# Performance work log

Measured on AMD Instinct MI355X. Metric: run time of the kernel, lower is better.

The kernel has to match this reference:

```python
import jax, jax.numpy as jnp
import numpy as np

N_ENT = 50000
N_REL = 500
N_EDGE = 800000
D_IN = 100
D_OUT = 100
ALPHA = 0.2  # LeakyReLU negative slope


def setup_inputs() -> dict:
    key = jax.random.key(0)
    k0, k1, k2, k3, k4 = jax.random.split(key, 5)
    entity_embedding = jax.random.normal(k0, (N_ENT, D_IN), dtype=jnp.float32) * 0.1
    relation_embedding = jax.random.normal(k1, (N_REL, D_IN), dtype=jnp.float32) * 0.1
    W = jax.random.normal(k2, (D_IN, D_OUT), dtype=jnp.float32) * 0.1
    edge_index = jax.random.randint(k3, (2, N_EDGE), 0, N_ENT, dtype=jnp.int32)
    edge_type = jax.random.randint(k4, (N_EDGE,), 0, N_REL, dtype=jnp.int32)
    return {
        "entity_embedding": entity_embedding,
        "relation_embedding": relation_embedding,
        "W": W,
        "edge_index": edge_index,
        "edge_type": edge_type,
    }


def reference(entity_embedding, relation_embedding, W, edge_index, edge_type):
    N = entity_embedding.shape[0]
    # project input embeddings with shared W (in_features -> out_features)
    ent = entity_embedding @ W          # [N_ent, D]
    rel = relation_embedding @ W        # [N_rel, D]

    h = edge_index[0]                   # destination / head nodes [E]
    t = edge_index[1]                   # source / tail nodes      [E]

    # TransE edge score: ||h + r - t||_2 per edge
    diff = ent[h] + rel[edge_type] - ent[t]          # [E, D]
    score = jnp.sqrt(jnp.sum(diff * diff, axis=1))   # [E]
    e = jax.nn.leaky_relu(score, negative_slope=ALPHA)

    # scatter-softmax over edges grouped by head node
    seg_max = jax.ops.segment_max(e, h, num_segments=N)         # [N]
    seg_max = jnp.where(jnp.isfinite(seg_max), seg_max, 0.0)    # empty segments -> -inf
    ex = jnp.exp(e - seg_max[h])                                 # [E]
    denom = jax.ops.segment_sum(ex, h, num_segments=N)          # [N]
    att = ex / (denom[h] + 1e-16)                                # [E]

    # message: composition 'sub' of tail embedding and relation, weighted by attention
    msg = (ent[t] - rel[edge_type]) * att[:, None]               # [E, D]
    out = jax.ops.segment_sum(msg, h, num_segments=N)            # [N, D]

    # concat=True -> nonlinearity (ELU, standard GAT behavior)
    return jax.nn.elu(out)
```

## Files before the change

kernel.cpp:

```cpp
#include <hip/hip_runtime.h>
#include <math.h>

#define N_ENT  50000
#define N_REL  500
#define N_EDGE 800000
#define D      100
#define ALPHA  0.2f

#define SCAN_B 256
#define NBLK_SCAN ((N_ENT + SCAN_B - 1) / SCAN_B)

#define PROJ_TPB  256
#define PROJ_RPB  50
#define ENT_BLKS  (N_ENT / PROJ_RPB)
#define REL_BLKS  (N_REL / PROJ_RPB)

__global__ __launch_bounds__(PROJ_TPB) void proj_kernel(const float* __restrict__ Xe,
                                                        const float* __restrict__ Xr,
                                                        const float* __restrict__ W,
                                                        float* __restrict__ Ye,
                                                        float* __restrict__ Yr,
                                                        int* __restrict__ deg) {
    __shared__ float Xs[PROJ_RPB * D];
    __shared__ float P[5][D];
    int t = threadIdx.x;

    const float* X; float* Y; size_t xbase;
    if (blockIdx.x < ENT_BLKS) {
        X = Xe; Y = Ye; xbase = (size_t)blockIdx.x * PROJ_RPB * D;
    } else {
        X = Xr; Y = Yr; xbase = (size_t)(blockIdx.x - ENT_BLKS) * PROJ_RPB * D;
    }

    int half, c;
    if (t < 100)                { half = 0; c = t; }
    else if (t >= 128 && t < 228) { half = 1; c = t - 128; }
    else                        { half = -1; c = 0; }

    if (half < 0) {
        int idx = (t < 128) ? (t - 100) : (28 + (t - 228));
        int j = blockIdx.x * 56 + idx;
        if (j < N_ENT) deg[j] = 0;
    }

    for (int i = t; i < PROJ_RPB * D; i += PROJ_TPB)
        Xs[i] = X[xbase + i];

    float w[52];
    if (half == 0) {
        #pragma unroll
        for (int k = 0; k < 52; ++k) w[k] = W[k * D + c];
    } else if (half == 1) {
        #pragma unroll
        for (int k = 0; k < 48; ++k) w[k] = W[(52 + k) * D + c];
    }
    __syncthreads();

    for (int g = 0; g < 10; ++g) {
        int r0 = g * 5;
        float a[5] = {0.f, 0.f, 0.f, 0.f, 0.f};
        if (half == 0) {
            #pragma unroll
            for (int r = 0; r < 5; ++r) {
                const float4* xr = (const float4*)&Xs[(r0 + r) * D];
                #pragma unroll
                for (int q = 0; q < 13; ++q) {
                    float4 xv = xr[q];
                    a[r] = fmaf(xv.x, w[4*q    ], a[r]);
                    a[r] = fmaf(xv.y, w[4*q + 1], a[r]);
                    a[r] = fmaf(xv.z, w[4*q + 2], a[r]);
                    a[r] = fmaf(xv.w, w[4*q + 3], a[r]);
                }
            }
        } else if (half == 1) {
            #pragma unroll
            for (int r = 0; r < 5; ++r) {
                const float4* xr = (const float4*)&Xs[(r0 + r) * D] + 13;
                #pragma unroll
                for (int q = 0; q < 12; ++q) {
                    float4 xv = xr[q];
                    a[r] = fmaf(xv.x, w[4*q    ], a[r]);
                    a[r] = fmaf(xv.y, w[4*q + 1], a[r]);
                    a[r] = fmaf(xv.z, w[4*q + 2], a[r]);
                    a[r] = fmaf(xv.w, w[4*q + 3], a[r]);
                }
            }
            #pragma unroll
            for (int r = 0; r < 5; ++r) P[r][c] = a[r];
        }
        __syncthreads();
        if (half == 0) {
            #pragma unroll
            for (int r = 0; r < 5; ++r)
                Y[xbase + (size_t)(r0 + r) * D + c] = a[r] + P[r][c];
        }
        __syncthreads();
    }
}

__global__ void degree_kernel(const int* __restrict__ h_idx, int* __restrict__ deg) {
    int e = blockIdx.x * blockDim.x + threadIdx.x;
    if (e < N_EDGE) atomicAdd(&deg[h_idx[e]], 1);
}

__global__ void scan1_kernel(const int* __restrict__ deg, int* __restrict__ bsum) {
    __shared__ int s[SCAN_B];
    int i = blockIdx.x * SCAN_B + threadIdx.x;
    s[threadIdx.x] = (i < N_ENT) ? deg[i] : 0;
    __syncthreads();
    for (int off = SCAN_B / 2; off; off >>= 1) {
        if (threadIdx.x < off) s[threadIdx.x] += s[threadIdx.x + off];
        __syncthreads();
    }
    if (threadIdx.x == 0) bsum[blockIdx.x] = s[0];
}

__global__ void scan2_kernel(const int* __restrict__ bsum, int* __restrict__ boff) {
    __shared__ int s[SCAN_B];
    int tid = threadIdx.x;
    int v = (tid < NBLK_SCAN) ? bsum[tid] : 0;
    s[tid] = v;
    __syncthreads();
    for (int off = 1; off < SCAN_B; off <<= 1) {
        int x = (tid >= off) ? s[tid - off] : 0;
        __syncthreads();
        s[tid] += x;
        __syncthreads();
    }
    if (tid < NBLK_SCAN) boff[tid] = s[tid] - v;
}

__global__ void scan3_kernel(const int* __restrict__ deg, const int* __restrict__ boff,
                             int* __restrict__ rowptr, int* __restrict__ cursor) {
    __shared__ int s[SCAN_B];
    int tid = threadIdx.x;
    int i = blockIdx.x * SCAN_B + tid;
    int v = (i < N_ENT) ? deg[i] : 0;
    s[tid] = v;
    __syncthreads();
    for (int off = 1; off < SCAN_B; off <<= 1) {
        int x = (tid >= off) ? s[tid - off] : 0;
        __syncthreads();
        s[tid] += x;
        __syncthreads();
    }
    int excl = s[tid] - v + boff[blockIdx.x];
    if (i < N_ENT) { rowptr[i] = excl; cursor[i] = excl; }
    if (i == N_ENT - 1) rowptr[N_ENT] = excl + v;
}

__global__ void fill_kernel(const int* __restrict__ h_idx, const int* __restrict__ t_idx,
                            const int* __restrict__ etype, int* __restrict__ cursor,
                            int2* __restrict__ tr_sorted) {
    int e = blockIdx.x * blockDim.x + threadIdx.x;
    if (e >= N_EDGE) return;
    int h = h_idx[e];
    int pos = atomicAdd(&cursor[h], 1);
    tr_sorted[pos] = make_int2(t_idx[e], etype[e]);
}

__device__ __forceinline__ float edge_reduce32(const float4& eh, const float4& v) {
    float dx = eh.x + v.x, dy = eh.y + v.y, dz = eh.z + v.z, dw = eh.w + v.w;
    float s = dx * dx;
    s = fmaf(dy, dy, s);
    s = fmaf(dz, dz, s);
    s = fmaf(dw, dw, s);
    #pragma unroll
    for (int off = 16; off; off >>= 1) s += __shfl_xor(s, off, 32);
    return sqrtf(s);
}

__device__ __forceinline__ void online_update(float sc, const float4& v,
                                              float& m, float& den, float4& acc) {
    float d  = sc - m;
    float e  = __expf(-fabsf(d));
    float scale = (d >= 0.f) ? e : 1.f;
    float ex    = (d >= 0.f) ? 1.f : e;
    m = fmaxf(m, sc);
    den   = den * scale + ex;
    acc.x = acc.x * scale - v.x * ex;
    acc.y = acc.y * scale - v.y * ex;
    acc.z = acc.z * scale - v.z * ex;
    acc.w = acc.w * scale - v.w * ex;
}

__global__ __launch_bounds__(256) void fused_kernel(const float* __restrict__ ent,
                                                    const float* __restrict__ rel,
                                                    const int* __restrict__ rowptr,
                                                    const int2* __restrict__ tr_sorted,
                                                    float* __restrict__ out) {
    int head = blockIdx.x * 8 + (threadIdx.x >> 5);
    int lane = threadIdx.x & 31;
    if (head >= N_ENT) return;
    int beg = rowptr[head], end = rowptr[head + 1];

    float4 eh = make_float4(0.f, 0.f, 0.f, 0.f);
    if (lane < 25) eh = ((const float4*)(ent + (size_t)head * D))[lane];

    float  m   = -INFINITY;
    float  den = 0.f;
    float4 acc = make_float4(0.f, 0.f, 0.f, 0.f);

    int i = beg;
    for (; i + 1 < end; i += 2) {
        int2 e0 = tr_sorted[i];
        int2 e1 = tr_sorted[i + 1];
        float4 v0 = make_float4(0.f, 0.f, 0.f, 0.f);
        float4 v1 = make_float4(0.f, 0.f, 0.f, 0.f);
        if (lane < 25) {
            float4 et0 = ((const float4*)(ent + (size_t)e0.x * D))[lane];
            float4 er0 = ((const float4*)(rel + (size_t)e0.y * D))[lane];
            float4 et1 = ((const float4*)(ent + (size_t)e1.x * D))[lane];
            float4 er1 = ((const float4*)(rel + (size_t)e1.y * D))[lane];
            v0 = make_float4(er0.x - et0.x, er0.y - et0.y, er0.z - et0.z, er0.w - et0.w);
            v1 = make_float4(er1.x - et1.x, er1.y - et1.y, er1.z - et1.z, er1.w - et1.w);
        }
        float sc0 = edge_reduce32(eh, v0);
        float sc1 = edge_reduce32(eh, v1);
        online_update(sc0, v0, m, den, acc);
        online_update(sc1, v1, m, den, acc);
    }
    if (i < end) {
        int2 e0 = tr_sorted[i];
        float4 v = make_float4(0.f, 0.f, 0.f, 0.f);
        if (lane < 25) {
            float4 et = ((const float4*)(ent + (size_t)e0.x * D))[lane];
            float4 er = ((const float4*)(rel + (size_t)e0.y * D))[lane];
            v = make_float4(er.x - et.x, er.y - et.y, er.z - et.z, er.w - et.w);
        }
        float sc = edge_reduce32(eh, v);
        online_update(sc, v, m, den, acc);
    }

    float inv = 1.f / (den + 1e-16f);
    float ox = acc.x * inv, oy = acc.y * inv, oz = acc.z * inv, ow = acc.w * inv;
    ox = ox > 0.f ? ox : expm1f(ox);
    oy = oy > 0.f ? oy : expm1f(oy);
    oz = oz > 0.f ? oz : expm1f(oz);
    ow = ow > 0.f ? ow : expm1f(ow);
    if (lane < 25)
        ((float4*)(out + (size_t)head * D))[lane] = make_float4(ox, oy, oz, ow);
}

extern "C" void kernel_launch(void* const* d_in, const int* in_sizes, int n_in,
                              void* d_out, int out_size, void* d_ws, size_t ws_size,
                              hipStream_t stream) {
    const float* entity_emb = (const float*)d_in[0];
    const float* rel_emb    = (const float*)d_in[1];
    const float* W          = (const float*)d_in[2];
    const int*   edge_index = (const int*)d_in[3];
    const int*   edge_type  = (const int*)d_in[4];
    float*       out        = (float*)d_out;

    const int* h_idx = edge_index;
    const int* t_idx = edge_index + N_EDGE;

    float* ent       = (float*)d_ws;
    float* rel       = ent + (size_t)N_ENT * D;
    int*   deg       = (int*)(rel + (size_t)N_REL * D);
    int*   rowptr    = deg + N_ENT;
    int*   cursor    = rowptr + (N_ENT + 1);
    int*   bsum      = cursor + N_ENT;
    int*   boff      = bsum + SCAN_B;
    int2*  tr_sorted = (int2*)(boff + SCAN_B);

    proj_kernel<<<ENT_BLKS + REL_BLKS, PROJ_TPB, 0, stream>>>(entity_emb, rel_emb,
                                                              W, ent, rel, deg);

    degree_kernel<<<(N_EDGE + 255) / 256, 256, 0, stream>>>(h_idx, deg);
    scan1_kernel<<<NBLK_SCAN, SCAN_B, 0, stream>>>(deg, bsum);
    scan2_kernel<<<1, SCAN_B, 0, stream>>>(bsum, boff);
    scan3_kernel<<<NBLK_SCAN, SCAN_B, 0, stream>>>(deg, boff, rowptr, cursor);
    fill_kernel<<<(N_EDGE + 255) / 256, 256, 0, stream>>>(h_idx, t_idx, edge_type,
                                                          cursor, tr_sorted);

    fused_kernel<<<N_ENT / 8, 256, 0, stream>>>(ent, rel, rowptr, tr_sorted, out);
}
```

Measured before the change: 266.2 us.

## Record per-edge rank during degree count, scatter edges without a second atomic pass

The degree-counting atomics now also save each edge's within-segment rank as a ushort, and this work is merged into the projection kernel as extra blocks. The CSR fill then computes each position as rowptr plus rank instead of doing a second atomicAdd on a cursor array, which removes the cursor writes and the fill-stage atomics. A memset replaces the in-kernel zeroing, adding a rank buffer read/write and relying on per-node degree staying under 65536. Edge order within a segment stays nondeterministic, as before.

```diff
diff --git a/kernel.cpp b/kernel.cpp
--- a/kernel.cpp
+++ b/kernel.cpp
@@ -14,16 +14,36 @@
 #define PROJ_RPB  50
 #define ENT_BLKS  (N_ENT / PROJ_RPB)
 #define REL_BLKS  (N_REL / PROJ_RPB)
-
-__global__ __launch_bounds__(PROJ_TPB) void proj_kernel(const float* __restrict__ Xe,
-                                                        const float* __restrict__ Xr,
-                                                        const float* __restrict__ W,
-                                                        float* __restrict__ Ye,
-                                                        float* __restrict__ Yr,
-                                                        int* __restrict__ deg) {
+#define PROJ_BLKS (ENT_BLKS + REL_BLKS)
+#define RANK_BLKS ((N_EDGE + 1023) / 1024)
+
+__global__ __launch_bounds__(PROJ_TPB) void proj_rank_kernel(const float* __restrict__ Xe,
+                                                             const float* __restrict__ Xr,
+                                                             const float* __restrict__ W,
+                                                             float* __restrict__ Ye,
+                                                             float* __restrict__ Yr,
+                                                             const int* __restrict__ h_idx,
+                                                             int* __restrict__ cnt,
+                                                             unsigned short* __restrict__ rank) {
+    int t = threadIdx.x;
+
+    if (blockIdx.x >= PROJ_BLKS) {
+        int eb = (blockIdx.x - PROJ_BLKS) * 1024 + t * 4;
+        if (eb + 3 < N_EDGE) {
+            int4 h4 = *(const int4*)(h_idx + eb);
+            rank[eb    ] = (unsigned short)atomicAdd(&cnt[h4.x], 1);
+            rank[eb + 1] = (unsigned short)atomicAdd(&cnt[h4.y], 1);
+            rank[eb + 2] = (unsigned short)atomicAdd(&cnt[h4.z], 1);
+            rank[eb + 3] = (unsigned short)atomicAdd(&cnt[h4.w], 1);
+        } else {
+            for (int e = eb; e < N_EDGE; ++e)
+                rank[e] = (unsigned short)atomicAdd(&cnt[h_idx[e]], 1);
+        }
+        return;
+    }
+
     __shared__ float Xs[PROJ_RPB * D];
     __shared__ float P[5][D];
-    int t = threadIdx.x;
 
     const float* X; float* Y; size_t xbase;
     if (blockIdx.x < ENT_BLKS) {
@@ -33,15 +53,9 @@
     }
 
     int half, c;
-    if (t < 100)                { half = 0; c = t; }
+    if (t < 100)                  { half = 0; c = t; }
     else if (t >= 128 && t < 228) { half = 1; c = t - 128; }
-    else                        { half = -1; c = 0; }
-
-    if (half < 0) {
-        int idx = (t < 128) ? (t - 100) : (28 + (t - 228));
-        int j = blockIdx.x * 56 + idx;
-        if (j < N_ENT) deg[j] = 0;
-    }
+    else                          { half = -1; c = 0; }
 
     for (int i = t; i < PROJ_RPB * D; i += PROJ_TPB)
         Xs[i] = X[xbase + i];
@@ -98,15 +112,10 @@
     }
 }
 
-__global__ void degree_kernel(const int* __restrict__ h_idx, int* __restrict__ deg) {
-    int e = blockIdx.x * blockDim.x + threadIdx.x;
-    if (e < N_EDGE) atomicAdd(&deg[h_idx[e]], 1);
-}
-
-__global__ void scan1_kernel(const int* __restrict__ deg, int* __restrict__ bsum) {
+__global__ void scan1_kernel(const int* __restrict__ cnt, int* __restrict__ bsum) {
     __shared__ int s[SCAN_B];
     int i = blockIdx.x * SCAN_B + threadIdx.x;
-    s[threadIdx.x] = (i < N_ENT) ? deg[i] : 0;
+    s[threadIdx.x] = (i < N_ENT) ? cnt[i] : 0;
     __syncthreads();
     for (int off = SCAN_B / 2; off; off >>= 1) {
         if (threadIdx.x < off) s[threadIdx.x] += s[threadIdx.x + off];
@@ -130,12 +139,12 @@
     if (tid < NBLK_SCAN) boff[tid] = s[tid] - v;
 }
 
-__global__ void scan3_kernel(const int* __restrict__ deg, const int* __restrict__ boff,
-                             int* __restrict__ rowptr, int* __restrict__ cursor) {
+__global__ void scan3_kernel(const int* __restrict__ cnt, const int* __restrict__ boff,
+                             int* __restrict__ rowptr) {
     __shared__ int s[SCAN_B];
     int tid = threadIdx.x;
     int i = blockIdx.x * SCAN_B + tid;
-    int v = (i < N_ENT) ? deg[i] : 0;
+    int v = (i < N_ENT) ? cnt[i] : 0;
     s[tid] = v;
     __syncthreads();
     for (int off = 1; off < SCAN_B; off <<= 1) {
@@ -145,17 +154,19 @@
         __syncthreads();
     }
     int excl = s[tid] - v + boff[blockIdx.x];
-    if (i < N_ENT) { rowptr[i] = excl; cursor[i] = excl; }
+    if (i < N_ENT) rowptr[i] = excl;
     if (i == N_ENT - 1) rowptr[N_ENT] = excl + v;
 }
 
-__global__ void fill_kernel(const int* __restrict__ h_idx, const int* __restrict__ t_idx,
-                            const int* __restrict__ etype, int* __restrict__ cursor,
-                            int2* __restrict__ tr_sorted) {
+__global__ void scatter_kernel(const int* __restrict__ h_idx, const int* __restrict__ t_idx,
+                               const int* __restrict__ etype,
+                               const int* __restrict__ rowptr,
+                               const unsigned short* __restrict__ rank,
+                               int2* __restrict__ tr_sorted) {
     int e = blockIdx.x * blockDim.x + threadIdx.x;
     if (e >= N_EDGE) return;
     int h = h_idx[e];
-    int pos = atomicAdd(&cursor[h], 1);
+    int pos = rowptr[h] + (int)rank[e];
     tr_sorted[pos] = make_int2(t_idx[e], etype[e]);
 }
 
@@ -255,24 +266,26 @@
     const int* h_idx = edge_index;
     const int* t_idx = edge_index + N_EDGE;
 
-    float* ent       = (float*)d_ws;
-    float* rel       = ent + (size_t)N_ENT * D;
-    int*   deg       = (int*)(rel + (size_t)N_REL * D);
-    int*   rowptr    = deg + N_ENT;
-    int*   cursor    = rowptr + (N_ENT + 1);
-    int*   bsum      = cursor + N_ENT;
-    int*   boff      = bsum + SCAN_B;
-    int2*  tr_sorted = (int2*)(boff + SCAN_B);
-
-    proj_kernel<<<ENT_BLKS + REL_BLKS, PROJ_TPB, 0, stream>>>(entity_emb, rel_emb,
-                                                              W, ent, rel, deg);
-
-    degree_kernel<<<(N_EDGE + 255) / 256, 256, 0, stream>>>(h_idx, deg);
-    scan1_kernel<<<NBLK_SCAN, SCAN_B, 0, stream>>>(deg, bsum);
+    float*          ent       = (float*)d_ws;
+    float*          rel       = ent + (size_t)N_ENT * D;
+    int*            cnt       = (int*)(rel + (size_t)N_REL * D);
+    int*            rowptr    = cnt + N_ENT;
+    int*            bsum      = rowptr + (N_ENT + 1);
+    int*            boff      = bsum + SCAN_B;
+    unsigned short* rank      = (unsigned short*)(boff + SCAN_B);
+    int2*           tr_sorted = (int2*)(rank + N_EDGE);
+
+    hipMemsetAsync(cnt, 0, N_ENT * sizeof(int), stream);
+
+    proj_rank_kernel<<<PROJ_BLKS + RANK_BLKS, PROJ_TPB, 0, stream>>>(
+        entity_emb, rel_emb, W, ent, rel, h_idx, cnt, rank);
+
+    scan1_kernel<<<NBLK_SCAN, SCAN_B, 0, stream>>>(cnt, bsum);
     scan2_kernel<<<1, SCAN_B, 0, stream>>>(bsum, boff);
-    scan3_kernel<<<NBLK_SCAN, SCAN_B, 0, stream>>>(deg, boff, rowptr, cursor);
-    fill_kernel<<<(N_EDGE + 255) / 256, 256, 0, stream>>>(h_idx, t_idx, edge_type,
-                                                          cursor, tr_sorted);
+    scan3_kernel<<<NBLK_SCAN, SCAN_B, 0, stream>>>(cnt, boff, rowptr);
+
+    scatter_kernel<<<(N_EDGE + 255) / 256, 256, 0, stream>>>(h_idx, t_idx, edge_type,
+                                                             rowptr, rank, tr_sorted);
 
     fused_kernel<<<N_ENT / 8, 256, 0, stream>>>(ent, rel, rowptr, tr_sorted, out);
 }
```

Result: faster. 228.9 us (-14.0%).
